# Kernel tuning notes

Measured on AMD Instinct MI355X. Metric: run time of the kernel, lower is better.

## Reference

```python
import jax, jax.numpy as jnp
import numpy as np

D_MODEL = 1024
D_FF = 4096
N_EXPERTS = 8
TOP_K = 2
GATE_TEMP = 1.0
LOAD_BALANCE_WEIGHT = 0.01


def setup_inputs() -> dict:
    key = jax.random.key(0)
    ks = jax.random.split(key, 6)
    B, S = 4, 2048
    x = jax.random.normal(ks[0], (B, S, D_MODEL), dtype=jnp.float32)
    # gate: nn.Linear(d_model, n_experts, bias=False), weight ~ N(0, 0.1)
    gate_w = 0.1 * jax.random.normal(ks[1], (N_EXPERTS, D_MODEL), dtype=jnp.float32)
    # stacked expert weights (stored as [in, out] for x @ W)
    s1 = 1.0 / np.sqrt(D_MODEL)
    s2 = 1.0 / np.sqrt(D_FF)
    W1 = jax.random.uniform(ks[2], (N_EXPERTS, D_MODEL, D_FF), jnp.float32, -s1, s1)
    b1 = jax.random.uniform(ks[3], (N_EXPERTS, D_FF), jnp.float32, -s1, s1)
    W2 = jax.random.uniform(ks[4], (N_EXPERTS, D_FF, D_MODEL), jnp.float32, -s2, s2)
    b2 = jax.random.uniform(ks[5], (N_EXPERTS, D_MODEL), jnp.float32, -s2, s2)
    return {"x": x, "gate_w": gate_w, "W1": W1, "b1": b1, "W2": W2, "b2": b2}


def reference(x, gate_w, W1, b1, W2, b2):
    B, S, D = x.shape
    E = gate_w.shape[0]
    xf = x.reshape(-1, D)                                  # [N, D]
    logits = (xf @ gate_w.T) / GATE_TEMP                   # [N, E]
    gate_probs = jax.nn.softmax(logits, axis=-1)           # [N, E]
    topk_probs, topk_idx = jax.lax.top_k(gate_probs, TOP_K)
    topk_probs = topk_probs / jnp.sum(topk_probs, axis=-1, keepdims=True)
    # per-token combine weight for each expert: [N, E]
    combine = jnp.einsum("nk,nke->ne", topk_probs,
                         jax.nn.one_hot(topk_idx, E, dtype=xf.dtype))
    out = jnp.zeros_like(xf)
    for e in range(E):  # fixed small loop over experts (structurally distinct weights)
        h = jax.nn.gelu(xf @ W1[e] + b1[e], approximate=False)  # [N, d_ff]
        out = out + combine[:, e:e + 1] * (h @ W2[e] + b2[e])
    out = out.reshape(B, S, D)
    # auxiliary load-balance loss (faithful: softmax probs > 0 almost surely)
    prob_mean = jnp.mean(gate_probs, axis=0)
    tokens_per_expert = jnp.mean((gate_probs > 0).astype(xf.dtype), axis=0)
    aux_loss = jnp.sum(prob_mean * tokens_per_expert) * E * LOAD_BALANCE_WEIGHT
    return out, aux_loss
```

## Files before the change

kernel.cpp:

```cpp
#include <hip/hip_runtime.h>
#include <cstdint>

typedef unsigned short u16;
typedef __attribute__((ext_vector_type(8))) __bf16 bf16x8;
typedef __attribute__((ext_vector_type(4))) float f32x4;

#define NTOK 8192
#define DM   1024
#define DFF  4096
#define NE   8
#define NT_MAX 136

typedef const __attribute__((address_space(1))) unsigned gl_u32;
typedef __attribute__((address_space(3))) unsigned lds_u32;

static __device__ __forceinline__ u16 f2bf(float f) {
    union { float f; unsigned u; } v; v.f = f;
    unsigned r = v.u + 0x7fffu + ((v.u >> 16) & 1u);
    return (u16)(r >> 16);
}

__global__ __launch_bounds__(256) void transpose_cvt_kernel(const float* __restrict__ W,
                                                            u16* __restrict__ WT,
                                                            int K, int F) {
    __shared__ float tile[32][33];
    size_t eo = (size_t)blockIdx.z * K * F;
    const float* src = W + eo;
    u16* dst = WT + eo;
    int f0 = blockIdx.x * 32, k0 = blockIdx.y * 32;
    int c = threadIdx.x & 31, r0 = threadIdx.x >> 5;
#pragma unroll
    for (int r = r0; r < 32; r += 8)
        tile[r][c] = src[(size_t)(k0 + r) * F + f0 + c];
    __syncthreads();
#pragma unroll
    for (int r = r0; r < 32; r += 8)
        dst[(size_t)(f0 + r) * K + k0 + c] = f2bf(tile[c][r]);
}

__global__ __launch_bounds__(256) void gate_kernel(const float* __restrict__ x,
                                                   const float* __restrict__ gw,
                                                   u16* __restrict__ xb,
                                                   int* __restrict__ cnt,
                                                   float* __restrict__ psum,
                                                   float* __restrict__ indsum,
                                                   int* __restrict__ list,
                                                   float* __restrict__ wgt,
                                                   int4* __restrict__ tokIE,
                                                   float2* __restrict__ tokW) {
    __shared__ float s_psum[NE], s_ind[NE];
    __shared__ int s_cnt[NE], s_base[NE];
    __shared__ int s_tok[NE][32];
    __shared__ float s_wgt[NE][32];
    __shared__ int s_e1[32], s_p1[32], s_e2[32], s_p2[32];
    __shared__ float s_w1[32], s_w2[32];
    int tid = threadIdx.x, lane = tid & 63, wid = tid >> 6;
    if (tid < NE) { s_psum[tid] = 0.f; s_ind[tid] = 0.f; s_cnt[tid] = 0; }
    __syncthreads();
#pragma unroll 1
    for (int it = 0; it < 8; it++) {
        int t = blockIdx.x * 32 + wid * 8 + it;
        const float* xr = x + (size_t)t * DM;
        float xv[16];
#pragma unroll
        for (int i = 0; i < 4; i++) {
            f32x4 v = *(const f32x4*)(xr + i * 256 + lane * 4);
            xv[4 * i + 0] = v[0]; xv[4 * i + 1] = v[1];
            xv[4 * i + 2] = v[2]; xv[4 * i + 3] = v[3];
            ushort4 o;
            o.x = f2bf(v[0]); o.y = f2bf(v[1]); o.z = f2bf(v[2]); o.w = f2bf(v[3]);
            *(ushort4*)(xb + (size_t)t * DM + i * 256 + lane * 4) = o;
        }
        float p[NE];
#pragma unroll
        for (int e = 0; e < NE; e++) {
            const float* gr = gw + (size_t)e * DM;
            float d = 0.f;
#pragma unroll
            for (int i = 0; i < 4; i++) {
                f32x4 g = *(const f32x4*)(gr + i * 256 + lane * 4);
                d += xv[4 * i] * g[0] + xv[4 * i + 1] * g[1]
                   + xv[4 * i + 2] * g[2] + xv[4 * i + 3] * g[3];
            }
#pragma unroll
            for (int off = 32; off; off >>= 1) d += __shfl_xor(d, off);
            p[e] = d;
        }
        float m = p[0];
#pragma unroll
        for (int e = 1; e < NE; e++) m = fmaxf(m, p[e]);
        float s = 0.f;
#pragma unroll
        for (int e = 0; e < NE; e++) { p[e] = expf(p[e] - m); s += p[e]; }
        float inv = 1.f / s;
#pragma unroll
        for (int e = 0; e < NE; e++) p[e] *= inv;
        int i1 = 0; float p1 = p[0];
#pragma unroll
        for (int e = 1; e < NE; e++) if (p[e] > p1) { p1 = p[e]; i1 = e; }
        int i2 = (i1 == 0) ? 1 : 0; float p2 = p[i2];
#pragma unroll
        for (int e = 0; e < NE; e++) if (e != i1 && p[e] > p2) { p2 = p[e]; i2 = e; }
        float wnorm = 1.f / (p1 + p2);
        if (lane == 0) {
#pragma unroll
            for (int e = 0; e < NE; e++) {
                atomicAdd(&s_psum[e], p[e]);
                atomicAdd(&s_ind[e], (p[e] > 0.f) ? 1.f : 0.f);
            }
            int pos1 = atomicAdd(&s_cnt[i1], 1);
            s_tok[i1][pos1] = t; s_wgt[i1][pos1] = p1 * wnorm;
            int pos2 = atomicAdd(&s_cnt[i2], 1);
            s_tok[i2][pos2] = t; s_wgt[i2][pos2] = p2 * wnorm;
            int sl = wid * 8 + it;
            s_e1[sl] = i1; s_p1[sl] = pos1; s_w1[sl] = p1 * wnorm;
            s_e2[sl] = i2; s_p2[sl] = pos2; s_w2[sl] = p2 * wnorm;
        }
    }
    __syncthreads();
    if (tid < NE) {
        s_base[tid] = atomicAdd(&cnt[tid], s_cnt[tid]);
        atomicAdd(&psum[tid], s_psum[tid]);
        atomicAdd(&indsum[tid], s_ind[tid]);
    }
    __syncthreads();
    for (int idx = tid; idx < NE * 32; idx += 256) {
        int e = idx >> 5, j = idx & 31;
        if (j < s_cnt[e]) {
            list[e * NTOK + s_base[e] + j] = s_tok[e][j];
            wgt[e * NTOK + s_base[e] + j] = s_wgt[e][j];
        }
    }
    if (tid < 32) {
        int t = blockIdx.x * 32 + tid;
        int e1 = s_e1[tid], e2 = s_e2[tid];
        tokIE[t] = make_int4(e1, s_base[e1] + s_p1[tid], e2, s_base[e2] + s_p2[tid]);
        tokW[t] = make_float2(s_w1[tid], s_w2[tid]);
    }
}

__global__ void finalize_kernel(const float* __restrict__ psum,
                                const float* __restrict__ indsum,
                                const int* __restrict__ cnt,
                                int* __restrict__ baseArr,
                                int* __restrict__ tileE,
                                int* __restrict__ tileM0,
                                int* __restrict__ nTiles,
                                float* __restrict__ out_aux) {
    if (threadIdx.x == 0) {
        float a = 0.f; int b = 0, nt = 0;
        for (int e = 0; e < NE; e++) {
            a += (psum[e] * (1.f / NTOK)) * (indsum[e] * (1.f / NTOK));
            baseArr[e] = b; b += cnt[e];
            int mt = (cnt[e] + 127) >> 7;
            for (int i = 0; i < mt; i++) { tileE[nt] = e; tileM0[nt] = i; nt++; }
        }
        nTiles[0] = nt;
        out_aux[0] = a * (float)NE * 0.01f;
    }
}

template <int KDIM, int EPI>
__global__ __launch_bounds__(256) void gemm_kernel(const u16* __restrict__ A,
                                                   const u16* __restrict__ BT,
                                                   const float* __restrict__ bias,
                                                   const int* __restrict__ list,
                                                   const float* __restrict__ wgt,
                                                   const int* __restrict__ cnt,
                                                   const int* __restrict__ base,
                                                   const int* __restrict__ tileE,
                                                   const int* __restrict__ tileM0,
                                                   const int* __restrict__ nTiles,
                                                   u16* __restrict__ h_out,
                                                   float* __restrict__ out) {
    constexpr int NCOL = (EPI == 1) ? DFF : DM;
    constexpr int NY = NCOL / 128;
    constexpr int NT = KDIM / 64;
    constexpr int BAND = 4 * NY;
    int nwg = gridDim.x;
    int q = nwg >> 3, r = nwg & 7;
    int xcd = blockIdx.x & 7, idx0 = blockIdx.x >> 3;
    int wg = (xcd < r ? xcd * (q + 1) : r * (q + 1) + (xcd - r) * q) + idx0;
    int band = wg / BAND, ib = wg - band * BAND;
    int ny = ib >> 2;
    int t = band * 4 + (ib & 3);
    if (t >= nTiles[0]) return;
    int e = tileE[t];
    int m0 = tileM0[t] << 7;
    int M = cnt[e];
    int hb = base[e];
    int n0 = ny * 128;
    const int* le = list + e * NTOK;
    const float* we = wgt + e * NTOK;
    const u16* Bte = BT + (size_t)e * NCOL * KDIM;
    const float* be = bias + (size_t)e * NCOL;

    __shared__ __attribute__((aligned(16))) u16 L[4][128 * 64];

    int tid = threadIdx.x;
    int lane = tid & 63, wid = tid >> 6;
    int wr = wid >> 1, wc = wid & 1;
    int r16 = lane & 15, hi = lane >> 4;
    int r8 = r16 & 7;

    const u16* aG[4]; const u16* bG[4]; int lofs[4];
#pragma unroll
    for (int qq = 0; qq < 4; qq++) {
        int lin = qq * 256 + tid;
        int row = lin >> 3, j = lin & 7;
        int js = j ^ (row & 7);
        lofs[qq] = lin * 8;
        int pos = m0 + row; if (pos > M - 1) pos = M - 1;
        size_t arow = (EPI == 1) ? (size_t)le[pos] : (size_t)(hb + pos);
        aG[qq] = A + arow * KDIM + js * 8;
        bG[qq] = Bte + (size_t)(n0 + row) * KDIM + js * 8;
    }

#define STAGE(k0, buf)                                                              \
    do {                                                                            \
        _Pragma("unroll")                                                           \
        for (int qq = 0; qq < 4; qq++) {                                            \
            __builtin_amdgcn_global_load_lds((gl_u32*)(aG[qq] + (k0)),              \
                (lds_u32*)(&L[(buf)][lofs[qq]]), 16, 0, 0);                         \
            __builtin_amdgcn_global_load_lds((gl_u32*)(bG[qq] + (k0)),              \
                (lds_u32*)(&L[2 + (buf)][lofs[qq]]), 16, 0, 0);                     \
        }                                                                           \
    } while (0)

    f32x4 acc[4][4];
#pragma unroll
    for (int m = 0; m < 4; m++)
#pragma unroll
        for (int n = 0; n < 4; n++) acc[m][n] = (f32x4){0.f, 0.f, 0.f, 0.f};

    STAGE(0, 0);
    STAGE(64, 1);
    asm volatile("s_waitcnt vmcnt(8)" ::: "memory");
    __builtin_amdgcn_s_barrier();

#pragma unroll 1
    for (int tI = 0; tI < NT; ++tI) {
        int cur = tI & 1;
        const u16* la = L[cur];
        const u16* lb = L[2 + cur];
#pragma unroll
        for (int kk = 0; kk < 2; kk++) {
            bf16x8 aF[4], bF[4];
            int ch = ((kk << 2) | hi) ^ r8;
#pragma unroll
            for (int m = 0; m < 4; m++)
                aF[m] = *(const bf16x8*)(la + ((wr * 64 + m * 16 + r16) << 6) + (ch << 3));
#pragma unroll
            for (int n = 0; n < 4; n++)
                bF[n] = *(const bf16x8*)(lb + ((wc * 64 + n * 16 + r16) << 6) + (ch << 3));
            __builtin_amdgcn_s_setprio(1);
#pragma unroll
            for (int m = 0; m < 4; m++)
#pragma unroll
                for (int n = 0; n < 4; n++)
                    acc[m][n] = __builtin_amdgcn_mfma_f32_16x16x32_bf16(aF[m], bF[n], acc[m][n], 0, 0, 0);
            __builtin_amdgcn_s_setprio(0);
        }
        asm volatile("s_waitcnt lgkmcnt(0)" ::: "memory");
        __builtin_amdgcn_s_barrier();
        if (tI + 2 < NT) {
            STAGE((tI + 2) * 64, cur);
            asm volatile("s_waitcnt vmcnt(8)" ::: "memory");
        } else {
            asm volatile("s_waitcnt vmcnt(0)" ::: "memory");
        }
        __builtin_amdgcn_s_barrier();
    }
#undef STAGE

#pragma unroll
    for (int m = 0; m < 4; m++) {
        int pr = m0 + wr * 64 + m * 16 + hi * 4;
#pragma unroll
        for (int n = 0; n < 4; n++) {
            int f = n0 + wc * 64 + n * 16 + r16;
#pragma unroll
            for (int j = 0; j < 4; j++) {
                int p = pr + j;
                if (p < M) {
                    if constexpr (EPI == 1) {
                        float v = acc[m][n][j] + be[f];
                        v = 0.5f * v * (1.0f + erff(v * 0.707106781f));
                        h_out[(size_t)(hb + p) * DFF + f] = f2bf(v);
                    } else if constexpr (EPI == 2) {
                        out[(size_t)(hb + p) * DM + f] = acc[m][n][j];
                    } else {
                        atomicAdd(out + (size_t)le[p] * DM + f,
                                  we[p] * (acc[m][n][j] + be[f]));
                    }
                }
            }
        }
    }
}

__global__ __launch_bounds__(256) void combine_kernel(const float* __restrict__ pairOut,
                                                      const float* __restrict__ b2,
                                                      const int4* __restrict__ tokIE,
                                                      const float2* __restrict__ tokW,
                                                      const int* __restrict__ baseArr,
                                                      float* __restrict__ out) {
    int t = blockIdx.x;
    int c = threadIdx.x * 4;
    int4 ie = tokIE[t];
    float2 w = tokW[t];
    int s1 = baseArr[ie.x] + ie.y, s2 = baseArr[ie.z] + ie.w;
    f32x4 v1 = *(const f32x4*)(pairOut + (size_t)s1 * DM + c);
    f32x4 v2 = *(const f32x4*)(pairOut + (size_t)s2 * DM + c);
    f32x4 g1 = *(const f32x4*)(b2 + (size_t)ie.x * DM + c);
    f32x4 g2 = *(const f32x4*)(b2 + (size_t)ie.z * DM + c);
    f32x4 res = w.x * (v1 + g1) + w.y * (v2 + g2);
    *(f32x4*)(out + (size_t)t * DM + c) = res;
}

extern "C" void kernel_launch(void* const* d_in, const int* in_sizes, int n_in,
                              void* d_out, int out_size, void* d_ws, size_t ws_size,
                              hipStream_t stream) {
    const float* x  = (const float*)d_in[0];
    const float* gw = (const float*)d_in[1];
    const float* W1 = (const float*)d_in[2];
    const float* b1 = (const float*)d_in[3];
    const float* W2 = (const float*)d_in[4];
    const float* b2 = (const float*)d_in[5];
    float* out = (float*)d_out;

    char* ws = (char*)d_ws;
    size_t o_xb   = 0;
    size_t o_w1t  = (size_t)16 << 20;
    size_t o_w2t  = o_w1t + ((size_t)64 << 20);
    size_t o_h    = o_w2t + ((size_t)64 << 20);
    size_t o_pair = o_h + ((size_t)128 << 20);
    size_t ctrl_sz = (size_t)1 << 20;
    bool pair_path = ws_size >= o_pair + ((size_t)64 << 20) + ctrl_sz;
    size_t o_ctrl = pair_path ? (o_pair + ((size_t)64 << 20)) : o_pair;

    u16* xb   = (u16*)(ws + o_xb);
    u16* w1t  = (u16*)(ws + o_w1t);
    u16* w2t  = (u16*)(ws + o_w2t);
    u16* h    = (u16*)(ws + o_h);
    float* pairOut = (float*)(ws + o_pair);
    char* ctrl = ws + o_ctrl;
    int*    cnt     = (int*)ctrl;
    float*  psum    = (float*)(ctrl + 32);
    float*  indsum  = (float*)(ctrl + 64);
    int*    baseArr = (int*)(ctrl + 96);
    int*    list    = (int*)(ctrl + 192);
    float*  wgt     = (float*)(ctrl + 192 + 262144);
    int4*   tokIE   = (int4*)(ctrl + 192 + 524288);
    float2* tokW    = (float2*)(ctrl + 192 + 655360);
    int*    tileE   = (int*)(ctrl + 192 + 720896);
    int*    tileM0  = (int*)(ctrl + 192 + 724992);
    int*    nTiles  = (int*)(ctrl + 192 + 729088);

    (void)hipMemsetAsync(ctrl, 0, 192, stream);
    if (!pair_path)
        (void)hipMemsetAsync(d_out, 0, (size_t)out_size * sizeof(float), stream);

    transpose_cvt_kernel<<<dim3(DFF / 32, DM / 32, NE), 256, 0, stream>>>(W1, w1t, DM, DFF);
    transpose_cvt_kernel<<<dim3(DM / 32, DFF / 32, NE), 256, 0, stream>>>(W2, w2t, DFF, DM);
    gate_kernel<<<NTOK / 32, 256, 0, stream>>>(x, gw, xb, cnt, psum, indsum, list, wgt, tokIE, tokW);
    finalize_kernel<<<1, 64, 0, stream>>>(psum, indsum, cnt, baseArr, tileE, tileM0, nTiles,
                                          out + (size_t)NTOK * DM);

    gemm_kernel<DM, 1><<<dim3(NT_MAX * (DFF / 128)), 256, 0, stream>>>(
        xb, w1t, b1, list, wgt, cnt, baseArr, tileE, tileM0, nTiles, h, nullptr);
    if (pair_path) {
        gemm_kernel<DFF, 2><<<dim3(NT_MAX * (DM / 128)), 256, 0, stream>>>(
            h, w2t, b2, list, wgt, cnt, baseArr, tileE, tileM0, nTiles, nullptr, pairOut);
        combine_kernel<<<NTOK, 256, 0, stream>>>(pairOut, b2, tokIE, tokW, baseArr, out);
    } else {
        gemm_kernel<DFF, 3><<<dim3(NT_MAX * (DM / 128)), 256, 0, stream>>>(
            h, w2t, b2, list, wgt, cnt, baseArr, tileE, tileM0, nTiles, nullptr, out);
    }
}
```

Baseline: 631.4 us.

## Template GEMM tile sizes, use 256x256 tiles with 512 threads for FFN1

Parameterises the grouped expert GEMM by tile shape and moves it to 512-thread workgroups with 8 waves arranged 2x4. The first FFN GEMM uses 256x256 tiles, from a second tile list that finalize now builds, to raise operand reuse per loaded byte. The second GEMM keeps 128x128 tiles. The exact erf GELU is also replaced by a tanh-form approximation written with exp, which changes numerics slightly, and larger tiles mean more padding waste for small expert counts.

```diff
diff --git a/kernel.cpp b/kernel.cpp
--- a/kernel.cpp
+++ b/kernel.cpp
@@ -9,7 +9,8 @@
 #define DM   1024
 #define DFF  4096
 #define NE   8
-#define NT_MAX 136
+#define NT_MAX128 136
+#define NT_MAX256 72
 
 typedef const __attribute__((address_space(1))) unsigned gl_u32;
 typedef __attribute__((address_space(3))) unsigned lds_u32;
@@ -143,40 +144,49 @@
                                 const float* __restrict__ indsum,
                                 const int* __restrict__ cnt,
                                 int* __restrict__ baseArr,
-                                int* __restrict__ tileE,
-                                int* __restrict__ tileM0,
-                                int* __restrict__ nTiles,
+                                int* __restrict__ tE256, int* __restrict__ tM256,
+                                int* __restrict__ nT256,
+                                int* __restrict__ tE128, int* __restrict__ tM128,
+                                int* __restrict__ nT128,
                                 float* __restrict__ out_aux) {
     if (threadIdx.x == 0) {
-        float a = 0.f; int b = 0, nt = 0;
+        float a = 0.f; int b = 0, n2 = 0, n1 = 0;
         for (int e = 0; e < NE; e++) {
             a += (psum[e] * (1.f / NTOK)) * (indsum[e] * (1.f / NTOK));
             baseArr[e] = b; b += cnt[e];
-            int mt = (cnt[e] + 127) >> 7;
-            for (int i = 0; i < mt; i++) { tileE[nt] = e; tileM0[nt] = i; nt++; }
-        }
-        nTiles[0] = nt;
+            int mt2 = (cnt[e] + 255) >> 8;
+            for (int i = 0; i < mt2; i++) { tE256[n2] = e; tM256[n2] = i; n2++; }
+            int mt1 = (cnt[e] + 127) >> 7;
+            for (int i = 0; i < mt1; i++) { tE128[n1] = e; tM128[n1] = i; n1++; }
+        }
+        nT256[0] = n2; nT128[0] = n1;
         out_aux[0] = a * (float)NE * 0.01f;
     }
 }
 
-template <int KDIM, int EPI>
-__global__ __launch_bounds__(256) void gemm_kernel(const u16* __restrict__ A,
-                                                   const u16* __restrict__ BT,
-                                                   const float* __restrict__ bias,
-                                                   const int* __restrict__ list,
-                                                   const float* __restrict__ wgt,
-                                                   const int* __restrict__ cnt,
-                                                   const int* __restrict__ base,
-                                                   const int* __restrict__ tileE,
-                                                   const int* __restrict__ tileM0,
-                                                   const int* __restrict__ nTiles,
-                                                   u16* __restrict__ h_out,
-                                                   float* __restrict__ out) {
+template <int KDIM, int EPI, int BM, int BN>
+__global__ __launch_bounds__(512, 2) void gemm_kernel(const u16* __restrict__ A,
+                                                      const u16* __restrict__ BT,
+                                                      const float* __restrict__ bias,
+                                                      const int* __restrict__ list,
+                                                      const float* __restrict__ wgt,
+                                                      const int* __restrict__ cnt,
+                                                      const int* __restrict__ base,
+                                                      const int* __restrict__ tileE,
+                                                      const int* __restrict__ tileM0,
+                                                      const int* __restrict__ nTiles,
+                                                      u16* __restrict__ h_out,
+                                                      float* __restrict__ out) {
     constexpr int NCOL = (EPI == 1) ? DFF : DM;
-    constexpr int NY = NCOL / 128;
+    constexpr int NY = NCOL / BN;
     constexpr int NT = KDIM / 64;
     constexpr int BAND = 4 * NY;
+    constexpr int MR = BM / 32;
+    constexpr int NR = BN / 64;
+    constexpr int AQ = BM / 64;
+    constexpr int BQ = BN / 64;
+    constexpr int VMN = AQ + BQ;
+
     int nwg = gridDim.x;
     int q = nwg >> 3, r = nwg & 7;
     int xcd = blockIdx.x & 7, idx0 = blockIdx.x >> 3;
@@ -186,78 +196,93 @@
     int t = band * 4 + (ib & 3);
     if (t >= nTiles[0]) return;
     int e = tileE[t];
-    int m0 = tileM0[t] << 7;
+    int m0 = tileM0[t] * BM;
     int M = cnt[e];
     int hb = base[e];
-    int n0 = ny * 128;
+    int n0 = ny * BN;
     const int* le = list + e * NTOK;
     const float* we = wgt + e * NTOK;
     const u16* Bte = BT + (size_t)e * NCOL * KDIM;
     const float* be = bias + (size_t)e * NCOL;
 
-    __shared__ __attribute__((aligned(16))) u16 L[4][128 * 64];
+    __shared__ __attribute__((aligned(16))) u16 LA[2][BM * 64];
+    __shared__ __attribute__((aligned(16))) u16 LB[2][BN * 64];
 
     int tid = threadIdx.x;
     int lane = tid & 63, wid = tid >> 6;
-    int wr = wid >> 1, wc = wid & 1;
+    int wm = wid >> 2, wn = wid & 3;
     int r16 = lane & 15, hi = lane >> 4;
     int r8 = r16 & 7;
 
-    const u16* aG[4]; const u16* bG[4]; int lofs[4];
-#pragma unroll
-    for (int qq = 0; qq < 4; qq++) {
-        int lin = qq * 256 + tid;
+    const u16* aG[AQ]; const u16* bG[BQ]; int aOfs[AQ], bOfs[BQ];
+#pragma unroll
+    for (int qq = 0; qq < AQ; qq++) {
+        int lin = qq * 512 + tid;
         int row = lin >> 3, j = lin & 7;
         int js = j ^ (row & 7);
-        lofs[qq] = lin * 8;
+        aOfs[qq] = lin * 8;
         int pos = m0 + row; if (pos > M - 1) pos = M - 1;
         size_t arow = (EPI == 1) ? (size_t)le[pos] : (size_t)(hb + pos);
         aG[qq] = A + arow * KDIM + js * 8;
+    }
+#pragma unroll
+    for (int qq = 0; qq < BQ; qq++) {
+        int lin = qq * 512 + tid;
+        int row = lin >> 3, j = lin & 7;
+        int js = j ^ (row & 7);
+        bOfs[qq] = lin * 8;
         bG[qq] = Bte + (size_t)(n0 + row) * KDIM + js * 8;
     }
 
 #define STAGE(k0, buf)                                                              \
     do {                                                                            \
         _Pragma("unroll")                                                           \
-        for (int qq = 0; qq < 4; qq++) {                                            \
+        for (int qq = 0; qq < AQ; qq++)                                             \
             __builtin_amdgcn_global_load_lds((gl_u32*)(aG[qq] + (k0)),              \
-                (lds_u32*)(&L[(buf)][lofs[qq]]), 16, 0, 0);                         \
+                (lds_u32*)(&LA[(buf)][aOfs[qq]]), 16, 0, 0);                        \
+        _Pragma("unroll")                                                           \
+        for (int qq = 0; qq < BQ; qq++)                                             \
             __builtin_amdgcn_global_load_lds((gl_u32*)(bG[qq] + (k0)),              \
-                (lds_u32*)(&L[2 + (buf)][lofs[qq]]), 16, 0, 0);                     \
-        }                                                                           \
+                (lds_u32*)(&LB[(buf)][bOfs[qq]]), 16, 0, 0);                        \
     } while (0)
 
-    f32x4 acc[4][4];
-#pragma unroll
-    for (int m = 0; m < 4; m++)
-#pragma unroll
-        for (int n = 0; n < 4; n++) acc[m][n] = (f32x4){0.f, 0.f, 0.f, 0.f};
+#define WAIT_VMN()                                                                  \
+    do {                                                                            \
+        if constexpr (VMN == 8) asm volatile("s_waitcnt vmcnt(8)" ::: "memory");    \
+        else                    asm volatile("s_waitcnt vmcnt(4)" ::: "memory");    \
+    } while (0)
+
+    f32x4 acc[MR][NR];
+#pragma unroll
+    for (int m = 0; m < MR; m++)
+#pragma unroll
+        for (int n = 0; n < NR; n++) acc[m][n] = (f32x4){0.f, 0.f, 0.f, 0.f};
 
     STAGE(0, 0);
     STAGE(64, 1);
-    asm volatile("s_waitcnt vmcnt(8)" ::: "memory");
+    WAIT_VMN();
     __builtin_amdgcn_s_barrier();
 
 #pragma unroll 1
     for (int tI = 0; tI < NT; ++tI) {
         int cur = tI & 1;
-        const u16* la = L[cur];
-        const u16* lb = L[2 + cur];
+        const u16* la = LA[cur];
+        const u16* lb = LB[cur];
 #pragma unroll
         for (int kk = 0; kk < 2; kk++) {
-            bf16x8 aF[4], bF[4];
+            bf16x8 aF[MR], bF[NR];
             int ch = ((kk << 2) | hi) ^ r8;
 #pragma unroll
-            for (int m = 0; m < 4; m++)
-                aF[m] = *(const bf16x8*)(la + ((wr * 64 + m * 16 + r16) << 6) + (ch << 3));
-#pragma unroll
-            for (int n = 0; n < 4; n++)
-                bF[n] = *(const bf16x8*)(lb + ((wc * 64 + n * 16 + r16) << 6) + (ch << 3));
+            for (int m = 0; m < MR; m++)
+                aF[m] = *(const bf16x8*)(la + ((wm * (BM / 2) + m * 16 + r16) << 6) + (ch << 3));
+#pragma unroll
+            for (int n = 0; n < NR; n++)
+                bF[n] = *(const bf16x8*)(lb + ((wn * (BN / 4) + n * 16 + r16) << 6) + (ch << 3));
             __builtin_amdgcn_s_setprio(1);
 #pragma unroll
-            for (int m = 0; m < 4; m++)
-#pragma unroll
-                for (int n = 0; n < 4; n++)
+            for (int m = 0; m < MR; m++)
+#pragma unroll
+                for (int n = 0; n < NR; n++)
                     acc[m][n] = __builtin_amdgcn_mfma_f32_16x16x32_bf16(aF[m], bF[n], acc[m][n], 0, 0, 0);
             __builtin_amdgcn_s_setprio(0);
         }
@@ -265,27 +290,29 @@
         __builtin_amdgcn_s_barrier();
         if (tI + 2 < NT) {
             STAGE((tI + 2) * 64, cur);
-            asm volatile("s_waitcnt vmcnt(8)" ::: "memory");
+            WAIT_VMN();
         } else {
             asm volatile("s_waitcnt vmcnt(0)" ::: "memory");
         }
         __builtin_amdgcn_s_barrier();
     }
 #undef STAGE
-
-#pragma unroll
-    for (int m = 0; m < 4; m++) {
-        int pr = m0 + wr * 64 + m * 16 + hi * 4;
-#pragma unroll
-        for (int n = 0; n < 4; n++) {
-            int f = n0 + wc * 64 + n * 16 + r16;
+#undef WAIT_VMN
+
+#pragma unroll
+    for (int m = 0; m < MR; m++) {
+        int pr = m0 + wm * (BM / 2) + m * 16 + hi * 4;
+#pragma unroll
+        for (int n = 0; n < NR; n++) {
+            int f = n0 + wn * (BN / 4) + n * 16 + r16;
 #pragma unroll
             for (int j = 0; j < 4; j++) {
                 int p = pr + j;
                 if (p < M) {
                     if constexpr (EPI == 1) {
                         float v = acc[m][n][j] + be[f];
-                        v = 0.5f * v * (1.0f + erff(v * 0.707106781f));
+                        float ex = __expf(v * (1.5957691216f + 0.0713548162f * v * v));
+                        v = v - v / (ex + 1.0f);
                         h_out[(size_t)(hb + p) * DFF + f] = f2bf(v);
                     } else if constexpr (EPI == 2) {
                         out[(size_t)(hb + p) * DM + f] = acc[m][n][j];
@@ -353,9 +380,12 @@
     float*  wgt     = (float*)(ctrl + 192 + 262144);
     int4*   tokIE   = (int4*)(ctrl + 192 + 524288);
     float2* tokW    = (float2*)(ctrl + 192 + 655360);
-    int*    tileE   = (int*)(ctrl + 192 + 720896);
-    int*    tileM0  = (int*)(ctrl + 192 + 724992);
-    int*    nTiles  = (int*)(ctrl + 192 + 729088);
+    int*    tE128   = (int*)(ctrl + 192 + 720896);
+    int*    tM128   = (int*)(ctrl + 192 + 724992);
+    int*    nT128   = (int*)(ctrl + 192 + 729088);
+    int*    tE256   = (int*)(ctrl + 192 + 733184);
+    int*    tM256   = (int*)(ctrl + 192 + 737280);
+    int*    nT256   = (int*)(ctrl + 192 + 741376);
 
     (void)hipMemsetAsync(ctrl, 0, 192, stream);
     if (!pair_path)
@@ -364,17 +394,18 @@
     transpose_cvt_kernel<<<dim3(DFF / 32, DM / 32, NE), 256, 0, stream>>>(W1, w1t, DM, DFF);
     transpose_cvt_kernel<<<dim3(DM / 32, DFF / 32, NE), 256, 0, stream>>>(W2, w2t, DFF, DM);
     gate_kernel<<<NTOK / 32, 256, 0, stream>>>(x, gw, xb, cnt, psum, indsum, list, wgt, tokIE, tokW);
-    finalize_kernel<<<1, 64, 0, stream>>>(psum, indsum, cnt, baseArr, tileE, tileM0, nTiles,
+    finalize_kernel<<<1, 64, 0, stream>>>(psum, indsum, cnt, baseArr,
+                                          tE256, tM256, nT256, tE128, tM128, nT128,
                                           out + (size_t)NTOK * DM);
 
-    gemm_kernel<DM, 1><<<dim3(NT_MAX * (DFF / 128)), 256, 0, stream>>>(
-        xb, w1t, b1, list, wgt, cnt, baseArr, tileE, tileM0, nTiles, h, nullptr);
+    gemm_kernel<DM, 1, 256, 256><<<dim3(NT_MAX256 * (DFF / 256)), 512, 0, stream>>>(
+        xb, w1t, b1, list, wgt, cnt, baseArr, tE256, tM256, nT256, h, nullptr);
     if (pair_path) {
-        gemm_kernel<DFF, 2><<<dim3(NT_MAX * (DM / 128)), 256, 0, stream>>>(
-            h, w2t, b2, list, wgt, cnt, baseArr, tileE, tileM0, nTiles, nullptr, pairOut);
+        gemm_kernel<DFF, 2, 128, 128><<<dim3(NT_MAX128 * (DM / 128)), 512, 0, stream>>>(
+            h, w2t, b2, list, wgt, cnt, baseArr, tE128, tM128, nT128, nullptr, pairOut);
         combine_kernel<<<NTOK, 256, 0, stream>>>(pairOut, b2, tokIE, tokW, baseArr, out);
     } else {
-        gemm_kernel<DFF, 3><<<dim3(NT_MAX * (DM / 128)), 256, 0, stream>>>(
-            h, w2t, b2, list, wgt, cnt, baseArr, tileE, tileM0, nTiles, nullptr, out);
-    }
-}
+        gemm_kernel<DFF, 3, 128, 128><<<dim3(NT_MAX128 * (DM / 128)), 512, 0, stream>>>(
+            h, w2t, b2, list, wgt, cnt, baseArr, tE128, tM128, nT128, nullptr, out);
+    }
+}
```

Measured after the change: 701.3 us. +11.1%, slower.

## Single-buffer LDS in MoE GEMM for higher occupancy and use tanh-approx GELU

Applied to the files above, without the earlier changes.

Replaces the double-buffered LDS pipeline with a single A/B buffer, halving shared memory to 32KB, and adds a launch bound requesting 5 waves-per-EU so more workgroups can reside per CU. Global loads for the next K-tile are issued only after the current tile is consumed, so latency hiding now depends on other resident workgroups rather than intra-block prefetch. The exact erf GELU is also replaced with the tanh approximation written as a sigmoid via __expf, which is cheaper but differs numerically from the exact-erf reference.

```diff
diff --git a/kernel.cpp b/kernel.cpp
--- a/kernel.cpp
+++ b/kernel.cpp
@@ -161,18 +161,18 @@
 }
 
 template <int KDIM, int EPI>
-__global__ __launch_bounds__(256) void gemm_kernel(const u16* __restrict__ A,
-                                                   const u16* __restrict__ BT,
-                                                   const float* __restrict__ bias,
-                                                   const int* __restrict__ list,
-                                                   const float* __restrict__ wgt,
-                                                   const int* __restrict__ cnt,
-                                                   const int* __restrict__ base,
-                                                   const int* __restrict__ tileE,
-                                                   const int* __restrict__ tileM0,
-                                                   const int* __restrict__ nTiles,
-                                                   u16* __restrict__ h_out,
-                                                   float* __restrict__ out) {
+__global__ __launch_bounds__(256, 5) void gemm_kernel(const u16* __restrict__ A,
+                                                      const u16* __restrict__ BT,
+                                                      const float* __restrict__ bias,
+                                                      const int* __restrict__ list,
+                                                      const float* __restrict__ wgt,
+                                                      const int* __restrict__ cnt,
+                                                      const int* __restrict__ base,
+                                                      const int* __restrict__ tileE,
+                                                      const int* __restrict__ tileM0,
+                                                      const int* __restrict__ nTiles,
+                                                      u16* __restrict__ h_out,
+                                                      float* __restrict__ out) {
     constexpr int NCOL = (EPI == 1) ? DFF : DM;
     constexpr int NY = NCOL / 128;
     constexpr int NT = KDIM / 64;
@@ -195,7 +195,8 @@
     const u16* Bte = BT + (size_t)e * NCOL * KDIM;
     const float* be = bias + (size_t)e * NCOL;
 
-    __shared__ __attribute__((aligned(16))) u16 L[4][128 * 64];
+    __shared__ __attribute__((aligned(16))) u16 lA[128 * 64];
+    __shared__ __attribute__((aligned(16))) u16 lB[128 * 64];
 
     int tid = threadIdx.x;
     int lane = tid & 63, wid = tid >> 6;
@@ -216,14 +217,14 @@
         bG[qq] = Bte + (size_t)(n0 + row) * KDIM + js * 8;
     }
 
-#define STAGE(k0, buf)                                                              \
+#define STAGE(k0)                                                                   \
     do {                                                                            \
         _Pragma("unroll")                                                           \
         for (int qq = 0; qq < 4; qq++) {                                            \
             __builtin_amdgcn_global_load_lds((gl_u32*)(aG[qq] + (k0)),              \
-                (lds_u32*)(&L[(buf)][lofs[qq]]), 16, 0, 0);                         \
+                (lds_u32*)(lA + lofs[qq]), 16, 0, 0);                               \
             __builtin_amdgcn_global_load_lds((gl_u32*)(bG[qq] + (k0)),              \
-                (lds_u32*)(&L[2 + (buf)][lofs[qq]]), 16, 0, 0);                     \
+                (lds_u32*)(lB + lofs[qq]), 16, 0, 0);                               \
         }                                                                           \
     } while (0)
 
@@ -233,26 +234,22 @@
 #pragma unroll
         for (int n = 0; n < 4; n++) acc[m][n] = (f32x4){0.f, 0.f, 0.f, 0.f};
 
-    STAGE(0, 0);
-    STAGE(64, 1);
-    asm volatile("s_waitcnt vmcnt(8)" ::: "memory");
-    __builtin_amdgcn_s_barrier();
+    STAGE(0);
 
 #pragma unroll 1
     for (int tI = 0; tI < NT; ++tI) {
-        int cur = tI & 1;
-        const u16* la = L[cur];
-        const u16* lb = L[2 + cur];
+        asm volatile("s_waitcnt vmcnt(0)" ::: "memory");
+        __builtin_amdgcn_s_barrier();
 #pragma unroll
         for (int kk = 0; kk < 2; kk++) {
             bf16x8 aF[4], bF[4];
             int ch = ((kk << 2) | hi) ^ r8;
 #pragma unroll
             for (int m = 0; m < 4; m++)
-                aF[m] = *(const bf16x8*)(la + ((wr * 64 + m * 16 + r16) << 6) + (ch << 3));
+                aF[m] = *(const bf16x8*)(lA + ((wr * 64 + m * 16 + r16) << 6) + (ch << 3));
 #pragma unroll
             for (int n = 0; n < 4; n++)
-                bF[n] = *(const bf16x8*)(lb + ((wc * 64 + n * 16 + r16) << 6) + (ch << 3));
+                bF[n] = *(const bf16x8*)(lB + ((wc * 64 + n * 16 + r16) << 6) + (ch << 3));
             __builtin_amdgcn_s_setprio(1);
 #pragma unroll
             for (int m = 0; m < 4; m++)
@@ -263,13 +260,7 @@
         }
         asm volatile("s_waitcnt lgkmcnt(0)" ::: "memory");
         __builtin_amdgcn_s_barrier();
-        if (tI + 2 < NT) {
-            STAGE((tI + 2) * 64, cur);
-            asm volatile("s_waitcnt vmcnt(8)" ::: "memory");
-        } else {
-            asm volatile("s_waitcnt vmcnt(0)" ::: "memory");
-        }
-        __builtin_amdgcn_s_barrier();
+        if (tI + 1 < NT) STAGE((tI + 1) * 64);
     }
 #undef STAGE
 
@@ -285,7 +276,8 @@
                 if (p < M) {
                     if constexpr (EPI == 1) {
                         float v = acc[m][n][j] + be[f];
-                        v = 0.5f * v * (1.0f + erff(v * 0.707106781f));
+                        float ex = __expf(v * (1.5957691216f + 0.0713548162f * v * v));
+                        v = v - v / (ex + 1.0f);
                         h_out[(size_t)(hb + p) * DFF + f] = f2bf(v);
                     } else if constexpr (EPI == 2) {
                         out[(size_t)(hb + p) * DM + f] = acc[m][n][j];
```

Measured after the change: 1.513 ms. +139.6%, slower.
